# Kernel optimization log

Measured on AMD Instinct MI355X. Metric: run time of the kernel, lower is better.

The kernel has to match this reference:

```python
import jax, jax.numpy as jnp
import numpy as np

B, L, A, C1, D, E = 1024, 26, 8192, 256, 512, 1024
THR = 1e-6

def setup_inputs() -> dict:
    key = jax.random.key(0)
    ks = jax.random.split(key, 12)
    s = 0.02
    return {
        "x": jax.random.normal(ks[0], (B, L, A), dtype=jnp.float32),
        "conv1_w": jax.random.normal(ks[1], (C1, A), dtype=jnp.float32) * s,
        "conv1_b": jax.random.normal(ks[2], (C1,), dtype=jnp.float32) * s,
        "conv2_w": jax.random.normal(ks[3], (D, C1), dtype=jnp.float32) * s,
        "conv2_b": jax.random.normal(ks[4], (D,), dtype=jnp.float32) * s,
        "w_ih": jax.random.normal(ks[5], (3 * D, D), dtype=jnp.float32) * s,
        "w_hh": jax.random.normal(ks[6], (3 * D, D), dtype=jnp.float32) * s,
        "b_ih": jax.random.normal(ks[7], (3 * D,), dtype=jnp.float32) * s,
        "b_hh": jax.random.normal(ks[8], (3 * D,), dtype=jnp.float32) * s,
        "lin_w": jax.random.normal(ks[9], (E, D), dtype=jnp.float32) * s,
        "lin_b": jax.random.normal(ks[10], (E,), dtype=jnp.float32) * s,
    }

def _threshold(v):
    # nn.Threshold(1e-6, 0): keep v where v > 1e-6, else 0
    return jnp.where(v > THR, v, jnp.zeros_like(v))

def reference(x, conv1_w, conv1_b, conv2_w, conv2_b, w_ih, w_hh, b_ih, b_hh, lin_w, lin_b):
    # 1x1 convs over length L == plain per-position GEMMs
    h = _threshold(jnp.einsum('bla,ca->blc', x, conv1_w) + conv1_b)      # [B,L,256]
    h = _threshold(jnp.einsum('blc,dc->bld', h, conv2_w) + conv2_b)      # [B,L,512]
    xs = jnp.swapaxes(h, 0, 1)                                           # [L,B,512]

    def gru_step(h_prev, x_t):
        gi = x_t @ w_ih.T + b_ih                                         # [B,3D]
        gh = h_prev @ w_hh.T + b_hh
        i_r, i_z, i_n = jnp.split(gi, 3, axis=-1)
        h_r, h_z, h_n = jnp.split(gh, 3, axis=-1)
        r = jax.nn.sigmoid(i_r + h_r)
        z = jax.nn.sigmoid(i_z + h_z)
        n = jnp.tanh(i_n + r * h_n)
        h_new = (1.0 - z) * n + z * h_prev
        return h_new, None

    h0 = jnp.zeros((x.shape[0], D), dtype=x.dtype)
    h_last, _ = jax.lax.scan(gru_step, h0, xs)                           # avg=False -> last hidden
    return h_last @ lin_w.T + lin_b                                      # [B,E]
```

## Files before the change

### kernel.cpp

```cpp
#include <hip/hip_runtime.h>

typedef __bf16 bf16;
typedef __bf16 bf16x8 __attribute__((ext_vector_type(8)));
typedef float f32x4 __attribute__((ext_vector_type(4)));

#define GLL16(gp, lp) __builtin_amdgcn_global_load_lds( \
    (__attribute__((address_space(1))) void*)(gp), \
    (__attribute__((address_space(3))) void*)(lp), 16, 0, 0)

__global__ void cvt_kernel(const float* __restrict__ src, bf16* __restrict__ dst, int n) {
    int i = blockIdx.x * 256 + threadIdx.x;
    if (i < n) dst[i] = (bf16)src[i];
}

__global__ void cvt_interleave_kernel(const float* __restrict__ src, bf16* __restrict__ dst) {
    int i = blockIdx.x * 256 + threadIdx.x;
    int row = i >> 9, c = i & 511;
    int g = row % 3, d = row / 3;
    dst[i] = (bf16)src[(g * 512 + d) * 512 + c];
}

__global__ __launch_bounds__(256) void conv1_kernel(
    const float* __restrict__ A, const bf16* __restrict__ B,
    const float* __restrict__ bias, bf16* __restrict__ out)
{
    const int K = 8192;
    __shared__ __align__(16) bf16 As[64 * 32];
    __shared__ __align__(16) bf16 Bs[256 * 32];
    const int tid = threadIdx.x;
    const int wave = tid >> 6, lane = tid & 63;
    const int quad = lane >> 4, l16 = lane & 15;
    const int wm = (wave & 1) * 32, wn = (wave >> 1) * 128;
    const int m0 = blockIdx.x * 64;
    const int ar = tid >> 2, akq = tid & 3;

    f32x4 acc[2][8] = {};
    const float* agp = A + (size_t)(m0 + ar) * K + akq * 8;

    for (int kt = 0; kt < K; kt += 32) {
        const float4* ap = (const float4*)(agp + kt);
        float4 p0 = ap[0], p1 = ap[1];
        bf16x8 v;
        v[0]=(bf16)p0.x; v[1]=(bf16)p0.y; v[2]=(bf16)p0.z; v[3]=(bf16)p0.w;
        v[4]=(bf16)p1.x; v[5]=(bf16)p1.y; v[6]=(bf16)p1.z; v[7]=(bf16)p1.w;
        *(bf16x8*)(As + tid * 8) = v;
        #pragma unroll
        for (int s = 0; s < 4; ++s) {
            int c = tid + s * 256;
            GLL16(B + (size_t)(c >> 2) * K + kt + (c & 3) * 8, Bs + c * 8);
        }
        __syncthreads();
        bf16x8 af[2], bfr[8];
        #pragma unroll
        for (int i = 0; i < 2; ++i)
            af[i] = *(const bf16x8*)(As + (wm + i * 16 + l16) * 32 + quad * 8);
        #pragma unroll
        for (int j = 0; j < 8; ++j)
            bfr[j] = *(const bf16x8*)(Bs + (wn + j * 16 + l16) * 32 + quad * 8);
        #pragma unroll
        for (int i = 0; i < 2; ++i)
            #pragma unroll
            for (int j = 0; j < 8; ++j)
                acc[i][j] = __builtin_amdgcn_mfma_f32_16x16x32_bf16(af[i], bfr[j], acc[i][j], 0, 0, 0);
        __syncthreads();
    }
    #pragma unroll
    for (int i = 0; i < 2; ++i)
        #pragma unroll
        for (int j = 0; j < 8; ++j)
            #pragma unroll
            for (int r = 0; r < 4; ++r) {
                int row = m0 + wm + i * 16 + quad * 4 + r;
                int col = wn + j * 16 + l16;
                float v2 = acc[i][j][r] + bias[col];
                v2 = (v2 > 1e-6f) ? v2 : 0.0f;
                out[(size_t)row * 256 + col] = (bf16)v2;
            }
}

__global__ __launch_bounds__(256) void gemm128_kernel(
    const bf16* __restrict__ A, const bf16* __restrict__ B,
    const float* __restrict__ bias, bf16* __restrict__ outh,
    float* __restrict__ outf, int M, int N, int K, int mode)
{
    __shared__ __align__(16) bf16 As[128 * 32];
    __shared__ __align__(16) bf16 Bs[128 * 32];
    const int tid = threadIdx.x;
    const int wave = tid >> 6, lane = tid & 63;
    const int quad = lane >> 4, l16 = lane & 15;
    const int wm = (wave & 1) * 64, wn = (wave >> 1) * 64;
    const int m0 = blockIdx.y * 128, n0 = blockIdx.x * 128;
    const int ar = tid >> 2, akq = tid & 3;

    f32x4 acc[4][4] = {};

    for (int kt = 0; kt < K; kt += 32) {
        GLL16(A + (size_t)(m0 + ar) * K + kt + akq * 8, As + tid * 8);
        GLL16(A + (size_t)(m0 + 64 + ar) * K + kt + akq * 8, As + 2048 + tid * 8);
        GLL16(B + (size_t)(n0 + ar) * K + kt + akq * 8, Bs + tid * 8);
        GLL16(B + (size_t)(n0 + 64 + ar) * K + kt + akq * 8, Bs + 2048 + tid * 8);
        __syncthreads();
        bf16x8 af[4], bfr[4];
        #pragma unroll
        for (int i = 0; i < 4; ++i) {
            af[i]  = *(const bf16x8*)(As + (wm + i * 16 + l16) * 32 + quad * 8);
            bfr[i] = *(const bf16x8*)(Bs + (wn + i * 16 + l16) * 32 + quad * 8);
        }
        #pragma unroll
        for (int i = 0; i < 4; ++i)
            #pragma unroll
            for (int j = 0; j < 4; ++j)
                acc[i][j] = __builtin_amdgcn_mfma_f32_16x16x32_bf16(af[i], bfr[j], acc[i][j], 0, 0, 0);
        __syncthreads();
    }
    #pragma unroll
    for (int i = 0; i < 4; ++i)
        #pragma unroll
        for (int j = 0; j < 4; ++j)
            #pragma unroll
            for (int r = 0; r < 4; ++r) {
                int row = m0 + wm + i * 16 + quad * 4 + r;
                int col = n0 + wn + j * 16 + l16;
                float v = acc[i][j][r];
                if (mode == 1) { int g = col % 3, d = col / 3; v += bias[g * 512 + d]; }
                else v += bias[col];
                if (mode == 0) v = (v > 1e-6f) ? v : 0.0f;
                if (mode == 2) outf[(size_t)row * N + col] = v;
                else outh[(size_t)row * N + col] = (bf16)v;
            }
}

__global__ __launch_bounds__(256) void gru_step_kernel(
    const bf16* __restrict__ gi,
    const bf16* __restrict__ whh,
    const float* __restrict__ bhh,
    const bf16* __restrict__ hprev,
    bf16* __restrict__ hout,
    int t, int first)
{
    const int K = 512;
    __shared__ __align__(16) char smem[64 * 100 * 4];
    bf16* As = (bf16*)smem;
    bf16* Bs = (bf16*)(smem + 4096);
    float* ghs = (float*)smem;

    const int tid = threadIdx.x;
    const int wave = tid >> 6, lane = tid & 63;
    const int quad = lane >> 4, l16 = lane & 15;
    const int wm = (wave & 1) * 32, wn = (wave >> 1) * 48;
    const int nb = blockIdx.x, mb = blockIdx.y;
    const int m0 = mb * 64, n0 = nb * 96;

    if (!first) {
        f32x4 acc[2][3] = {};
        const int ar = tid >> 2, akq = tid & 3;
        for (int kt = 0; kt < K; kt += 32) {
            GLL16(hprev + (size_t)(m0 + ar) * K + kt + akq * 8, As + tid * 8);
            GLL16(whh + (size_t)(n0 + ar) * K + kt + akq * 8, Bs + tid * 8);
            if (tid < 128) {
                int c = 256 + tid;
                GLL16(whh + (size_t)(n0 + (c >> 2)) * K + kt + (c & 3) * 8, Bs + c * 8);
            }
            __syncthreads();
            bf16x8 af[2], bfr[3];
            #pragma unroll
            for (int i = 0; i < 2; ++i)
                af[i] = *(const bf16x8*)(As + (wm + i * 16 + l16) * 32 + quad * 8);
            #pragma unroll
            for (int j = 0; j < 3; ++j)
                bfr[j] = *(const bf16x8*)(Bs + (wn + j * 16 + l16) * 32 + quad * 8);
            #pragma unroll
            for (int i = 0; i < 2; ++i)
                #pragma unroll
                for (int j = 0; j < 3; ++j)
                    acc[i][j] = __builtin_amdgcn_mfma_f32_16x16x32_bf16(af[i], bfr[j], acc[i][j], 0, 0, 0);
            __syncthreads();
        }
        #pragma unroll
        for (int i = 0; i < 2; ++i)
            #pragma unroll
            for (int j = 0; j < 3; ++j)
                #pragma unroll
                for (int r = 0; r < 4; ++r) {
                    int lrow = wm + i * 16 + quad * 4 + r;
                    int lcol = wn + j * 16 + l16;
                    int g = lcol % 3;
                    int dg = nb * 32 + lcol / 3;
                    ghs[lrow * 100 + lcol] = acc[i][j][r] + bhh[g * 512 + dg];
                }
    }
    __syncthreads();

    for (int it = 0; it < 8; ++it) {
        int item = it * 256 + tid;
        int lrow = item >> 5, ld = item & 31;
        int b = m0 + lrow;
        int dg = nb * 32 + ld;
        float ghr, ghz, ghn;
        if (first) { ghr = bhh[dg]; ghz = bhh[512 + dg]; ghn = bhh[1024 + dg]; }
        else {
            ghr = ghs[lrow * 100 + ld * 3];
            ghz = ghs[lrow * 100 + ld * 3 + 1];
            ghn = ghs[lrow * 100 + ld * 3 + 2];
        }
        size_t gb = ((size_t)b * 26 + t) * 1536 + n0 + ld * 3;
        float gir = (float)gi[gb], giz = (float)gi[gb + 1], gin = (float)gi[gb + 2];
        float hp = first ? 0.0f : (float)hprev[(size_t)b * 512 + dg];
        float rr = 1.0f / (1.0f + __expf(-(gir + ghr)));
        float zz = 1.0f / (1.0f + __expf(-(giz + ghz)));
        float nn = tanhf(gin + rr * ghn);
        hout[(size_t)b * 512 + dg] = (bf16)((1.0f - zz) * nn + zz * hp);
    }
}

extern "C" void kernel_launch(void* const* d_in, const int* in_sizes, int n_in,
                              void* d_out, int out_size, void* d_ws, size_t ws_size,
                              hipStream_t stream) {
    const float* x       = (const float*)d_in[0];
    const float* conv1_w = (const float*)d_in[1];
    const float* conv1_b = (const float*)d_in[2];
    const float* conv2_w = (const float*)d_in[3];
    const float* conv2_b = (const float*)d_in[4];
    const float* w_ih    = (const float*)d_in[5];
    const float* w_hh    = (const float*)d_in[6];
    const float* b_ih    = (const float*)d_in[7];
    const float* b_hh    = (const float*)d_in[8];
    const float* lin_w   = (const float*)d_in[9];
    const float* lin_b   = (const float*)d_in[10];
    float* out = (float*)d_out;

    bf16* ws   = (bf16*)d_ws;
    bf16* w1   = ws;
    bf16* w2   = w1  + 2097152;
    bf16* wih  = w2  + 131072;
    bf16* whh  = wih + 786432;
    bf16* wlin = whh + 786432;
    bf16* h1   = wlin + 524288;
    bf16* h2   = h1  + 6815744;
    bf16* gib  = h2  + 13631488;
    bf16* H0   = gib + 40894464;
    bf16* H1   = H0  + 524288;

    cvt_kernel<<<8192, 256, 0, stream>>>(conv1_w, w1, 2097152);
    cvt_kernel<<<512, 256, 0, stream>>>(conv2_w, w2, 131072);
    cvt_interleave_kernel<<<3072, 256, 0, stream>>>(w_ih, wih);
    cvt_interleave_kernel<<<3072, 256, 0, stream>>>(w_hh, whh);
    cvt_kernel<<<2048, 256, 0, stream>>>(lin_w, wlin, 524288);

    conv1_kernel<<<416, 256, 0, stream>>>(x, w1, conv1_b, h1);
    gemm128_kernel<<<dim3(4, 208), 256, 0, stream>>>(h1, w2, conv2_b, h2, nullptr, 26624, 512, 256, 0);
    gemm128_kernel<<<dim3(12, 208), 256, 0, stream>>>(h2, wih, b_ih, gib, nullptr, 26624, 1536, 512, 1);
    for (int t = 0; t < 26; ++t) {
        const bf16* hp = (t & 1) ? H1 : H0;
        bf16* ho = (t & 1) ? H0 : H1;
        gru_step_kernel<<<dim3(16, 16), 256, 0, stream>>>(gib, whh, b_hh, hp, ho, t, t == 0);
    }
    gemm128_kernel<<<dim3(8, 8), 256, 0, stream>>>(H0, wlin, lin_b, nullptr, out, 1024, 1024, 512, 2);
}
```

Measured before the change: 1.743 ms.

## Split-K conv1, fuse weight conversions, cache W_hh slice in LDS for GRU step

Conv1 is split four ways along K, so 1664 blocks run instead of 416, and a separate reduce kernel adds the fp32 partials, applies bias and threshold, and writes bf16. The five weight conversions become one launch, and the gate interleave is dropped in favour of a planar gate layout. The GRU step loads its whole W_hh slice into padded LDS once and reads h_prev directly from global memory, removing the per-K-tile syncs, and tanh is replaced with an exp-based form. The trade-off is the extra fp32 partial-buffer traffic for conv1 and about 100KB of LDS per GRU block, which limits occupancy.

```diff
diff --git a/kernel.cpp b/kernel.cpp
--- a/kernel.cpp
+++ b/kernel.cpp
@@ -2,27 +2,29 @@
 
 typedef __bf16 bf16;
 typedef __bf16 bf16x8 __attribute__((ext_vector_type(8)));
+typedef __bf16 bf16x4 __attribute__((ext_vector_type(4)));
 typedef float f32x4 __attribute__((ext_vector_type(4)));
 
 #define GLL16(gp, lp) __builtin_amdgcn_global_load_lds( \
     (__attribute__((address_space(1))) void*)(gp), \
     (__attribute__((address_space(3))) void*)(lp), 16, 0, 0)
 
-__global__ void cvt_kernel(const float* __restrict__ src, bf16* __restrict__ dst, int n) {
+__global__ void cvt_all_kernel(const float* __restrict__ a, const float* __restrict__ b,
+                               const float* __restrict__ c, const float* __restrict__ d,
+                               const float* __restrict__ e, bf16* __restrict__ dst) {
     int i = blockIdx.x * 256 + threadIdx.x;
-    if (i < n) dst[i] = (bf16)src[i];
-}
-
-__global__ void cvt_interleave_kernel(const float* __restrict__ src, bf16* __restrict__ dst) {
-    int i = blockIdx.x * 256 + threadIdx.x;
-    int row = i >> 9, c = i & 511;
-    int g = row % 3, d = row / 3;
-    dst[i] = (bf16)src[(g * 512 + d) * 512 + c];
+    float v;
+    if      (i < 2097152) v = a[i];
+    else if (i < 2228224) v = b[i - 2097152];
+    else if (i < 3014656) v = c[i - 2228224];
+    else if (i < 3801088) v = d[i - 3014656];
+    else if (i < 4325376) v = e[i - 3801088];
+    else return;
+    dst[i] = (bf16)v;
 }
 
 __global__ __launch_bounds__(256) void conv1_kernel(
-    const float* __restrict__ A, const bf16* __restrict__ B,
-    const float* __restrict__ bias, bf16* __restrict__ out)
+    const float* __restrict__ A, const bf16* __restrict__ B, float* __restrict__ P)
 {
     const int K = 8192;
     __shared__ __align__(16) bf16 As[64 * 32];
@@ -32,12 +34,13 @@
     const int quad = lane >> 4, l16 = lane & 15;
     const int wm = (wave & 1) * 32, wn = (wave >> 1) * 128;
     const int m0 = blockIdx.x * 64;
+    const int k0 = blockIdx.y * 2048;
     const int ar = tid >> 2, akq = tid & 3;
 
     f32x4 acc[2][8] = {};
     const float* agp = A + (size_t)(m0 + ar) * K + akq * 8;
 
-    for (int kt = 0; kt < K; kt += 32) {
+    for (int kt = k0; kt < k0 + 2048; kt += 32) {
         const float4* ap = (const float4*)(agp + kt);
         float4 p0 = ap[0], p1 = ap[1];
         bf16x8 v;
@@ -64,6 +67,7 @@
                 acc[i][j] = __builtin_amdgcn_mfma_f32_16x16x32_bf16(af[i], bfr[j], acc[i][j], 0, 0, 0);
         __syncthreads();
     }
+    float* Pp = P + (size_t)blockIdx.y * 26624 * 256;
     #pragma unroll
     for (int i = 0; i < 2; ++i)
         #pragma unroll
@@ -72,10 +76,28 @@
             for (int r = 0; r < 4; ++r) {
                 int row = m0 + wm + i * 16 + quad * 4 + r;
                 int col = wn + j * 16 + l16;
-                float v2 = acc[i][j][r] + bias[col];
-                v2 = (v2 > 1e-6f) ? v2 : 0.0f;
-                out[(size_t)row * 256 + col] = (bf16)v2;
+                Pp[(size_t)row * 256 + col] = acc[i][j][r];
             }
+}
+
+__global__ void conv1_reduce_kernel(const float* __restrict__ P, const float* __restrict__ bias,
+                                    bf16* __restrict__ out) {
+    const size_t plane = 26624ull * 256 / 4;
+    size_t i = blockIdx.x * 256 + threadIdx.x;
+    const float4* p = (const float4*)P;
+    float4 s0 = p[i], s1 = p[i + plane], s2 = p[i + 2 * plane], s3 = p[i + 3 * plane];
+    int col = (int)((i * 4) & 255);
+    float4 bb = *(const float4*)(bias + col);
+    float r0 = s0.x + s1.x + s2.x + s3.x + bb.x;
+    float r1 = s0.y + s1.y + s2.y + s3.y + bb.y;
+    float r2 = s0.z + s1.z + s2.z + s3.z + bb.z;
+    float r3 = s0.w + s1.w + s2.w + s3.w + bb.w;
+    bf16x4 o;
+    o[0] = (bf16)(r0 > 1e-6f ? r0 : 0.0f);
+    o[1] = (bf16)(r1 > 1e-6f ? r1 : 0.0f);
+    o[2] = (bf16)(r2 > 1e-6f ? r2 : 0.0f);
+    o[3] = (bf16)(r3 > 1e-6f ? r3 : 0.0f);
+    *(bf16x4*)(out + i * 4) = o;
 }
 
 __global__ __launch_bounds__(256) void gemm128_kernel(
@@ -121,9 +143,7 @@
             for (int r = 0; r < 4; ++r) {
                 int row = m0 + wm + i * 16 + quad * 4 + r;
                 int col = n0 + wn + j * 16 + l16;
-                float v = acc[i][j][r];
-                if (mode == 1) { int g = col % 3, d = col / 3; v += bias[g * 512 + d]; }
-                else v += bias[col];
+                float v = acc[i][j][r] + bias[col];
                 if (mode == 0) v = (v > 1e-6f) ? v : 0.0f;
                 if (mode == 2) outf[(size_t)row * N + col] = v;
                 else outh[(size_t)row * N + col] = (bf16)v;
@@ -138,44 +158,54 @@
     bf16* __restrict__ hout,
     int t, int first)
 {
-    const int K = 512;
-    __shared__ __align__(16) char smem[64 * 100 * 4];
-    bf16* As = (bf16*)smem;
-    bf16* Bs = (bf16*)(smem + 4096);
-    float* ghs = (float*)smem;
-
+    __shared__ __align__(16) char smem[99840];
     const int tid = threadIdx.x;
     const int wave = tid >> 6, lane = tid & 63;
     const int quad = lane >> 4, l16 = lane & 15;
     const int wm = (wave & 1) * 32, wn = (wave >> 1) * 48;
     const int nb = blockIdx.x, mb = blockIdx.y;
-    const int m0 = mb * 64, n0 = nb * 96;
+    const int m0 = mb * 64;
+    float* ghs = (float*)smem;
 
     if (!first) {
+        bf16* ws = (bf16*)smem;
+        bf16x8 tmp[24];
+        #pragma unroll
+        for (int ii = 0; ii < 24; ++ii) {
+            int cc = ii * 256 + tid;
+            int row = cc >> 6;
+            int col = (cc & 63) * 8;
+            int gr = (row < 32) ? nb * 32 + row
+                   : (row < 64) ? 512 + nb * 32 + (row - 32)
+                                : 1024 + nb * 32 + (row - 64);
+            tmp[ii] = *(const bf16x8*)(whh + (size_t)gr * 512 + col);
+        }
+        #pragma unroll
+        for (int ii = 0; ii < 24; ++ii) {
+            int cc = ii * 256 + tid;
+            int row = cc >> 6;
+            int col = (cc & 63) * 8;
+            *(bf16x8*)(ws + row * 520 + col) = tmp[ii];
+        }
+        __syncthreads();
+
         f32x4 acc[2][3] = {};
-        const int ar = tid >> 2, akq = tid & 3;
-        for (int kt = 0; kt < K; kt += 32) {
-            GLL16(hprev + (size_t)(m0 + ar) * K + kt + akq * 8, As + tid * 8);
-            GLL16(whh + (size_t)(n0 + ar) * K + kt + akq * 8, Bs + tid * 8);
-            if (tid < 128) {
-                int c = 256 + tid;
-                GLL16(whh + (size_t)(n0 + (c >> 2)) * K + kt + (c & 3) * 8, Bs + c * 8);
-            }
-            __syncthreads();
+        #pragma unroll
+        for (int kt = 0; kt < 512; kt += 32) {
             bf16x8 af[2], bfr[3];
             #pragma unroll
             for (int i = 0; i < 2; ++i)
-                af[i] = *(const bf16x8*)(As + (wm + i * 16 + l16) * 32 + quad * 8);
+                af[i] = *(const bf16x8*)(hprev + (size_t)(m0 + wm + i * 16 + l16) * 512 + kt + quad * 8);
             #pragma unroll
             for (int j = 0; j < 3; ++j)
-                bfr[j] = *(const bf16x8*)(Bs + (wn + j * 16 + l16) * 32 + quad * 8);
+                bfr[j] = *(const bf16x8*)(ws + (wn + j * 16 + l16) * 520 + kt + quad * 8);
             #pragma unroll
             for (int i = 0; i < 2; ++i)
                 #pragma unroll
                 for (int j = 0; j < 3; ++j)
                     acc[i][j] = __builtin_amdgcn_mfma_f32_16x16x32_bf16(af[i], bfr[j], acc[i][j], 0, 0, 0);
-            __syncthreads();
-        }
+        }
+        __syncthreads();
         #pragma unroll
         for (int i = 0; i < 2; ++i)
             #pragma unroll
@@ -184,31 +214,32 @@
                 for (int r = 0; r < 4; ++r) {
                     int lrow = wm + i * 16 + quad * 4 + r;
                     int lcol = wn + j * 16 + l16;
-                    int g = lcol % 3;
-                    int dg = nb * 32 + lcol / 3;
-                    ghs[lrow * 100 + lcol] = acc[i][j][r] + bhh[g * 512 + dg];
+                    int plane = lcol >> 5, dl = lcol & 31;
+                    ghs[lrow * 100 + lcol] = acc[i][j][r] + bhh[plane * 512 + nb * 32 + dl];
                 }
-    }
-    __syncthreads();
-
+        __syncthreads();
+    }
+
+    #pragma unroll
     for (int it = 0; it < 8; ++it) {
         int item = it * 256 + tid;
         int lrow = item >> 5, ld = item & 31;
         int b = m0 + lrow;
         int dg = nb * 32 + ld;
-        float ghr, ghz, ghn;
-        if (first) { ghr = bhh[dg]; ghz = bhh[512 + dg]; ghn = bhh[1024 + dg]; }
+        float ghr, ghz, ghn, hp;
+        if (first) { ghr = bhh[dg]; ghz = bhh[512 + dg]; ghn = bhh[1024 + dg]; hp = 0.0f; }
         else {
-            ghr = ghs[lrow * 100 + ld * 3];
-            ghz = ghs[lrow * 100 + ld * 3 + 1];
-            ghn = ghs[lrow * 100 + ld * 3 + 2];
-        }
-        size_t gb = ((size_t)b * 26 + t) * 1536 + n0 + ld * 3;
-        float gir = (float)gi[gb], giz = (float)gi[gb + 1], gin = (float)gi[gb + 2];
-        float hp = first ? 0.0f : (float)hprev[(size_t)b * 512 + dg];
+            ghr = ghs[lrow * 100 + ld];
+            ghz = ghs[lrow * 100 + 32 + ld];
+            ghn = ghs[lrow * 100 + 64 + ld];
+            hp  = (float)hprev[(size_t)b * 512 + dg];
+        }
+        size_t gb = ((size_t)b * 26 + t) * 1536;
+        float gir = (float)gi[gb + dg], giz = (float)gi[gb + 512 + dg], gin = (float)gi[gb + 1024 + dg];
         float rr = 1.0f / (1.0f + __expf(-(gir + ghr)));
         float zz = 1.0f / (1.0f + __expf(-(giz + ghz)));
-        float nn = tanhf(gin + rr * ghn);
+        float xx = gin + rr * ghn;
+        float nn = 1.0f - 2.0f / (__expf(2.0f * xx) + 1.0f);
         hout[(size_t)b * 512 + dg] = (bf16)((1.0f - zz) * nn + zz * hp);
     }
 }
@@ -229,8 +260,9 @@
     const float* lin_b   = (const float*)d_in[10];
     float* out = (float*)d_out;
 
-    bf16* ws   = (bf16*)d_ws;
-    bf16* w1   = ws;
+    float* P   = (float*)d_ws;
+    bf16* wsb  = (bf16*)(P + 4ull * 26624 * 256);
+    bf16* w1   = wsb;
     bf16* w2   = w1  + 2097152;
     bf16* wih  = w2  + 131072;
     bf16* whh  = wih + 786432;
@@ -241,13 +273,10 @@
     bf16* H0   = gib + 40894464;
     bf16* H1   = H0  + 524288;
 
-    cvt_kernel<<<8192, 256, 0, stream>>>(conv1_w, w1, 2097152);
-    cvt_kernel<<<512, 256, 0, stream>>>(conv2_w, w2, 131072);
-    cvt_interleave_kernel<<<3072, 256, 0, stream>>>(w_ih, wih);
-    cvt_interleave_kernel<<<3072, 256, 0, stream>>>(w_hh, whh);
-    cvt_kernel<<<2048, 256, 0, stream>>>(lin_w, wlin, 524288);
-
-    conv1_kernel<<<416, 256, 0, stream>>>(x, w1, conv1_b, h1);
+    cvt_all_kernel<<<16896, 256, 0, stream>>>(conv1_w, conv2_w, w_ih, w_hh, lin_w, w1);
+
+    conv1_kernel<<<dim3(416, 4), 256, 0, stream>>>(x, w1, P);
+    conv1_reduce_kernel<<<6656, 256, 0, stream>>>(P, conv1_b, h1);
     gemm128_kernel<<<dim3(4, 208), 256, 0, stream>>>(h1, w2, conv2_b, h2, nullptr, 26624, 512, 256, 0);
     gemm128_kernel<<<dim3(12, 208), 256, 0, stream>>>(h2, wih, b_ih, gib, nullptr, 26624, 1536, 512, 1);
     for (int t = 0; t < 26; ++t) {
```

Measured after the change: 1.728 ms. No clear change (-0.9%).
